# Performance work log

Measured on AMD Instinct MI355X. Metric: run time of the kernel, lower is better.

## Reference

```python
import jax, jax.numpy as jnp
import numpy as np

B = 128      # graphs in batch
NPG = 128    # nodes per graph
F = 256      # num_node_features
D = 192      # d_model
NH = 8       # decoder heads
L = 4        # decoder layers
DFF = 512
DEG = 16     # avg degree
P = 32       # num_patch_nodes
EH = 96      # encoder_hidden = max(D//2, 48)
GH = 4       # GAT heads (layer 1)
EPS = 1e-5


def _init(key, shape, fan_in):
    return jax.random.normal(key, shape, jnp.float32) / np.sqrt(fan_in)


def setup_inputs() -> dict:
    key = jax.random.key(0)
    ks = jax.random.split(key, 40)
    N = B * NPG
    E = N * DEG
    off = jnp.repeat(jnp.arange(B, dtype=jnp.int32) * NPG, E // B)
    src = jax.random.randint(ks[1], (E,), 0, NPG, dtype=jnp.int32) + off
    dst = jax.random.randint(ks[2], (E,), 0, NPG, dtype=jnp.int32) + off
    inp = dict(
        subgraph_x=jax.random.normal(ks[0], (N, F), jnp.float32),
        subgraph_edge_index=jnp.stack([src, dst]),
        target_local_idx=jax.random.randint(ks[3], (B,), 0, NPG, dtype=jnp.int32),
        batch=jnp.repeat(jnp.arange(B, dtype=jnp.int32), NPG),
        num_patch_nodes=P,
    )
    # GAT encoder params (PyG GATConv layout: W [heads*out, in], att [heads, out])
    inp['gat1_w'] = _init(ks[4], (GH * EH, F), F)
    inp['gat1_att_src'] = _init(ks[5], (GH, EH), EH)
    inp['gat1_att_dst'] = _init(ks[6], (GH, EH), EH)
    inp['gat1_b'] = jnp.zeros((GH * EH,), jnp.float32)
    inp['gat2_w'] = _init(ks[7], (D, GH * EH), GH * EH)
    inp['gat2_att_src'] = _init(ks[8], (1, D), D)
    inp['gat2_att_dst'] = _init(ks[9], (1, D), D)
    inp['gat2_b'] = jnp.zeros((D,), jnp.float32)
    # TransformerDecoder layers (stacked over L)
    inp['sa_qkv_w'] = _init(ks[10], (L, 3 * D, D), D)
    inp['sa_qkv_b'] = jnp.zeros((L, 3 * D), jnp.float32)
    inp['sa_out_w'] = _init(ks[11], (L, D, D), D)
    inp['sa_out_b'] = jnp.zeros((L, D), jnp.float32)
    inp['ca_qkv_w'] = _init(ks[12], (L, 3 * D, D), D)
    inp['ca_qkv_b'] = jnp.zeros((L, 3 * D), jnp.float32)
    inp['ca_out_w'] = _init(ks[13], (L, D, D), D)
    inp['ca_out_b'] = jnp.zeros((L, D), jnp.float32)
    inp['ff1_w'] = _init(ks[14], (L, DFF, D), D)
    inp['ff1_b'] = jnp.zeros((L, DFF), jnp.float32)
    inp['ff2_w'] = _init(ks[15], (L, D, DFF), DFF)
    inp['ff2_b'] = jnp.zeros((L, D), jnp.float32)
    inp['ln_g'] = jnp.ones((L, 3, D), jnp.float32)
    inp['ln_b'] = jnp.zeros((L, 3, D), jnp.float32)
    # feature head
    inp['h1_w'] = _init(ks[16], (D, D), D)
    inp['h1_b'] = jnp.zeros((D,), jnp.float32)
    inp['h2_w'] = _init(ks[17], (F, D), D)
    inp['h2_b'] = jnp.zeros((F,), jnp.float32)
    return inp


def _gat(x, src, dst, W, a_src, a_dst, bias, heads, ch, concat):
    # PyG GATConv with add_self_loops=True, negative_slope=0.2, eval mode (no dropout)
    N = x.shape[0]
    xp = (x @ W.T).reshape(N, heads, ch)
    loop = jnp.arange(N, dtype=src.dtype)
    s = jnp.concatenate([src, loop])
    d = jnp.concatenate([dst, loop])
    al_s = (xp * a_src).sum(-1)  # [N, H]
    al_d = (xp * a_dst).sum(-1)
    e = jax.nn.leaky_relu(al_s[s] + al_d[d], 0.2)  # [E+N, H]
    emax = jax.ops.segment_max(e, d, num_segments=N)
    ex = jnp.exp(e - emax[d])
    den = jax.ops.segment_sum(ex, d, num_segments=N)
    coef = ex / (den[d] + 1e-16)
    out = jax.ops.segment_sum(xp[s] * coef[:, :, None], d, num_segments=N)  # [N,H,C]
    out = out.reshape(N, heads * ch) if concat else out.mean(1)
    return out + bias


def _ln(x, g, b):
    m = x.mean(-1, keepdims=True)
    v = ((x - m) ** 2).mean(-1, keepdims=True)
    return (x - m) / jnp.sqrt(v + EPS) * g + b


def _mha(q_in, kv_in, qkv_w, qkv_b, out_w, out_b, causal):
    b, sq, d = q_in.shape
    sk = kv_in.shape[1]
    dh = d // NH
    wq, wk, wv = jnp.split(qkv_w, 3, axis=0)
    bq, bk, bv = jnp.split(qkv_b, 3)
    q = (q_in @ wq.T + bq).reshape(b, sq, NH, dh).transpose(0, 2, 1, 3)
    k = (kv_in @ wk.T + bk).reshape(b, sk, NH, dh).transpose(0, 2, 1, 3)
    v = (kv_in @ wv.T + bv).reshape(b, sk, NH, dh).transpose(0, 2, 1, 3)
    sc = jnp.einsum('bhqd,bhkd->bhqk', q, k) / np.sqrt(dh).astype(np.float32)
    if causal:
        sc = jnp.where(jnp.tril(jnp.ones((sq, sk), bool)), sc, -1e30)
    a = jax.nn.softmax(sc, axis=-1)
    o = jnp.einsum('bhqk,bhkd->bhqd', a, v).transpose(0, 2, 1, 3).reshape(b, sq, d)
    return o @ out_w.T + out_b


def _pe(max_len, d):
    pos = jnp.arange(max_len, dtype=jnp.float32)[:, None]
    div = jnp.exp(jnp.arange(0, d, 2, dtype=jnp.float32) * (-np.log(10000.0) / d))
    pe = jnp.zeros((max_len, d), jnp.float32)
    return pe.at[:, 0::2].set(jnp.sin(pos * div)).at[:, 1::2].set(jnp.cos(pos * div))


def _forward(subgraph_x, gat1_w, gat1_att_src, gat1_att_dst, gat1_b,
             gat2_w, gat2_att_src, gat2_att_dst, gat2_b,
             sa_qkv_w, sa_qkv_b, sa_out_w, sa_out_b,
             ca_qkv_w, ca_qkv_b, ca_out_w, ca_out_b,
             ff1_w, ff1_b, ff2_w, ff2_b, ln_g, ln_b,
             h1_w, h1_b, h2_w, h2_b,
             subgraph_edge_index, target_local_idx, batch, num_patch_nodes):
    src, dst = subgraph_edge_index[0], subgraph_edge_index[1]
    h = jax.nn.elu(_gat(subgraph_x, src, dst, gat1_w, gat1_att_src, gat1_att_dst, gat1_b, GH, EH, True))
    mem = _gat(h, src, dst, gat2_w, gat2_att_src, gat2_att_dst, gat2_b, 1, D, False)
    bsz = target_local_idx.shape[0]
    mem_d = mem.reshape(bsz, -1, D)  # to_dense_batch: equal-sized, sorted graphs -> reshape, mask all-valid
    tgt = mem_d[jnp.arange(bsz), target_local_idx][:, None, :]  # [B,1,D]
    Pn = int(num_patch_nodes)
    pe = _pe(Pn + 1, D)
    feats = []
    adj = jnp.zeros((bsz, Pn + 1, Pn + 1), subgraph_x.dtype)
    for i in range(Pn):
        s = i + 1
        x = tgt + pe[None, :s]  # pos encoding (dropout is eval no-op)
        for l in range(L):
            x = _ln(x + _mha(x, x, sa_qkv_w[l], sa_qkv_b[l], sa_out_w[l], sa_out_b[l], True), ln_g[l, 0], ln_b[l, 0])
            x = _ln(x + _mha(x, mem_d, ca_qkv_w[l], ca_qkv_b[l], ca_out_w[l], ca_out_b[l], False), ln_g[l, 1], ln_b[l, 1])
            ff = jax.nn.gelu(x @ ff1_w[l].T + ff1_b[l], approximate=False) @ ff2_w[l].T + ff2_b[l]
            x = _ln(x + ff, ln_g[l, 2], ln_b[l, 2])
        last = x[:, -1]  # [B,D]
        feats.append(jax.nn.gelu(last @ h1_w.T + h1_b, approximate=False) @ h2_w.T + h2_b)
        cl = jnp.einsum('bsd,bd->bs', x, last)  # connection logits, len s
        adj = adj.at[:, i, Pn].set(cl[:, 0]).at[:, Pn, i].set(cl[:, 0])
        if i > 0:
            adj = adj.at[:, i, :i].set(cl[:, 1:i + 1]).at[:, :i, i].set(cl[:, 1:i + 1])
        tgt = jnp.concatenate([tgt, jax.lax.stop_gradient(last)[:, None]], axis=1)  # .detach() in torch
    adj = jnp.triu(adj, 1)
    adj = adj + jnp.swapaxes(adj, -1, -2)  # symmetric, zero diagonal
    return jnp.stack(feats, axis=1), adj


def reference(subgraph_x, subgraph_edge_index, target_local_idx, batch, num_patch_nodes,
              gat1_w, gat1_att_src, gat1_att_dst, gat1_b,
              gat2_w, gat2_att_src, gat2_att_dst, gat2_b,
              sa_qkv_w, sa_qkv_b, sa_out_w, sa_out_b,
              ca_qkv_w, ca_qkv_b, ca_out_w, ca_out_b,
              ff1_w, ff1_b, ff2_w, ff2_b, ln_g, ln_b,
              h1_w, h1_b, h2_w, h2_b):
    return _forward(subgraph_x, gat1_w, gat1_att_src, gat1_att_dst, gat1_b,
                    gat2_w, gat2_att_src, gat2_att_dst, gat2_b,
                    sa_qkv_w, sa_qkv_b, sa_out_w, sa_out_b,
                    ca_qkv_w, ca_qkv_b, ca_out_w, ca_out_b,
                    ff1_w, ff1_b, ff2_w, ff2_b, ln_g, ln_b,
                    h1_w, h1_b, h2_w, h2_b,
                    subgraph_edge_index, target_local_idx, batch, num_patch_nodes)
```

## Files before the change

### kernel.cpp

```cpp
#include <hip/hip_runtime.h>
#include <hip/hip_bf16.h>
#include <math.h>

#define DEV __device__ __forceinline__
typedef unsigned int u32;
typedef unsigned short u16;

constexpr int NNODES = 16384;
constexpr int NEDGE  = 262144;
constexpr int NEL    = NEDGE + NNODES;
constexpr int FIN    = 256;
constexpr int C1     = 384;
constexpr int DM     = 192;
constexpr int BZ     = 128;
constexpr int NPG_   = 128;
constexpr int LL     = 4;
constexpr int PP     = 32;
constexpr int SM     = 33;
constexpr int DFF_   = 512;

constexpr int PL4     = 52224;
constexpr int OFF4_QKV = 0;
constexpr int OFF4_SAO = 13824;
constexpr int OFF4_CAQ = 18432;
constexpr int OFF4_CAO = 23040;
constexpr int OFF4_FF1 = 27648;
constexpr int OFF4_FF2 = 39936;
constexpr int OFF4_H1  = 4*PL4;
constexpr int OFF4_H2  = OFF4_H1 + 4608;

constexpr size_t O_KVK = 0;
constexpr size_t O_VT  = 6291456;
constexpr size_t O_XP1 = 0;
constexpr size_t O_H   = 6291456;
constexpr size_t O_XP2 = 12582912;
constexpr size_t O_MEM = 15728640;
constexpr size_t O_WP  = 20545536;
constexpr size_t O_PE  = 21424128;
constexpr size_t O_AL1S= O_PE + 6336;
constexpr size_t O_AL1D= O_AL1S + 65536;
constexpr size_t O_AL2S= O_AL1D + 65536;
constexpr size_t O_AL2D= O_AL2S + 16384;
constexpr size_t O_CNT = O_AL2D + 16384;
constexpr size_t O_BASE= O_CNT + 16384;
constexpr size_t O_FILL= O_BASE + 16384;
constexpr size_t O_CSRC= O_FILL + 16384;

DEV float gelu_f(float v) { return 0.5f*v*(1.0f + erff(v*0.7071067811865475f)); }
DEV float bflo(u32 w) { return __uint_as_float(w << 16); }
DEV float bfhi(u32 w) { return __uint_as_float(w & 0xffff0000u); }
DEV float bfu(u16 u)  { return __uint_as_float(((u32)u) << 16); }
DEV u16 bf16u(float a) {
  __hip_bfloat16 h = __float2bfloat16(a);
  return *reinterpret_cast<u16*>(&h);
}
DEV u32 pk2(float a, float b) {
  return (u32)bf16u(a) | ((u32)bf16u(b) << 16);
}
DEV void fma8(float& a, uint4 w, float4 xa, float4 xb) {
  a = fmaf(bflo(w.x), xa.x, a); a = fmaf(bfhi(w.x), xa.y, a);
  a = fmaf(bflo(w.y), xa.z, a); a = fmaf(bfhi(w.y), xa.w, a);
  a = fmaf(bflo(w.z), xb.x, a); a = fmaf(bfhi(w.z), xb.y, a);
  a = fmaf(bflo(w.w), xb.z, a); a = fmaf(bfhi(w.w), xb.w, a);
}
template<int NU4, int STRIDE>
DEV float dotcol(const uint4* __restrict__ col, const float* __restrict__ xv) {
  const float4* x4 = (const float4*)xv;
  float a0 = 0, a1 = 0, a2 = 0, a3 = 0;
  #pragma unroll
  for (int q = 0; q < NU4; ++q) {
    uint4 w = col[(size_t)q*STRIDE];
    if ((q & 3) == 0) fma8(a0, w, x4[2*q], x4[2*q+1]);
    else if ((q & 3) == 1) fma8(a1, w, x4[2*q], x4[2*q+1]);
    else if ((q & 3) == 2) fma8(a2, w, x4[2*q], x4[2*q+1]);
    else fma8(a3, w, x4[2*q], x4[2*q+1]);
  }
  return (a0+a1)+(a2+a3);
}
template<int N> struct WB { uint4 w[N]; };
template<int N, int STRIDE>
DEV void wissue(WB<N>& r, const uint4* __restrict__ col) {
  #pragma unroll
  for (int q = 0; q < N; ++q) r.w[q] = col[(size_t)q*STRIDE];
}
template<int N>
DEV float wuse(const WB<N>& r, const float* __restrict__ xv) {
  const float4* x4 = (const float4*)xv;
  float a0 = 0, a1 = 0, a2 = 0, a3 = 0;
  #pragma unroll
  for (int q = 0; q < N; ++q) {
    float4 xa = x4[2*q], xb = x4[2*q+1];
    if ((q & 3) == 0) fma8(a0, r.w[q], xa, xb);
    else if ((q & 3) == 1) fma8(a1, r.w[q], xa, xb);
    else if ((q & 3) == 2) fma8(a2, r.w[q], xa, xb);
    else fma8(a3, r.w[q], xa, xb);
  }
  return (a0+a1)+(a2+a3);
}

__global__ void zero_kernel(float* adj, int* cnt, int* fill) {
  int i = blockIdx.x*256 + threadIdx.x;
  if (i < BZ*SM*SM) adj[i] = 0.f;
  if (i < NNODES) { cnt[i] = 0; fill[i] = 0; }
}

__global__ void pe_kernel(float* pe) {
  int idx = blockIdx.x*256 + threadIdx.x;
  if (idx >= SM*DM) return;
  int p = idx / DM, d = idx % DM;
  int i2 = d >> 1;
  float div = __expf((float)(2*i2) * (-9.210340371976184f / (float)DM));
  float a = (float)p * div;
  pe[idx] = (d & 1) ? cosf(a) : sinf(a);
}

__global__ void pack_kernel(const float* __restrict__ W, uint4* __restrict__ P, int N, int K) {
  int idx = blockIdx.x*256 + threadIdx.x;
  if (idx >= N*(K>>3)) return;
  int o = idx % N, kq = idx / N;
  const float* r = W + (size_t)o*K + 8*kq;
  uint4 u;
  u.x = pk2(r[0], r[1]); u.y = pk2(r[2], r[3]);
  u.z = pk2(r[4], r[5]); u.w = pk2(r[6], r[7]);
  P[idx] = u;
}

template<int BMODE, bool BF16OUT>
__global__ __launch_bounds__(256) void gemm_nt(const float* __restrict__ A,
    const float* __restrict__ W, const float* __restrict__ bias,
    float* __restrict__ Cf, __hip_bfloat16* __restrict__ Cb, int M, int N, int K)
{
  __shared__ float As[16][68];
  __shared__ float Ws[16][68];
  const int bm = blockIdx.y*64, bn = blockIdx.x*64;
  const int t = threadIdx.x, tx = t & 15, ty = t >> 4;
  float acc[4][4] = {};
  for (int k0 = 0; k0 < K; k0 += 16) {
    #pragma unroll
    for (int i = 0; i < 4; ++i) {
      int idx = t + i*256, kk = idx & 15, m = idx >> 4;
      As[kk][m] = A[(size_t)(bm+m)*K + k0+kk];
      Ws[kk][m] = W[(size_t)(bn+m)*K + k0+kk];
    }
    __syncthreads();
    #pragma unroll
    for (int kk = 0; kk < 16; ++kk) {
      const float4 a4 = *(const float4*)&As[kk][ty*4];
      const float4 b4 = *(const float4*)&Ws[kk][tx*4];
      const float av[4] = {a4.x,a4.y,a4.z,a4.w};
      const float bv[4] = {b4.x,b4.y,b4.z,b4.w};
      #pragma unroll
      for (int i = 0; i < 4; ++i)
        #pragma unroll
        for (int j = 0; j < 4; ++j)
          acc[i][j] = fmaf(av[i], bv[j], acc[i][j]);
    }
    __syncthreads();
  }
  #pragma unroll
  for (int i = 0; i < 4; ++i) {
    const int m = bm + ty*4 + i;
    #pragma unroll
    for (int j = 0; j < 4; ++j) {
      const int n = bn + tx*4 + j;
      float v = acc[i][j];
      if (BMODE == 1) v += bias[n];
      if (BMODE == 2) v += bias[m];
      if (BF16OUT) Cb[(size_t)m*N + n] = __float2bfloat16(v);
      else         Cf[(size_t)m*N + n] = v;
    }
  }
}

template<int HEADS, int CH>
__global__ void al_kernel(const float* __restrict__ xp, const float* __restrict__ asrc,
                          const float* __restrict__ adst, float* als, float* ald) {
  int idx = blockIdx.x*256 + threadIdx.x;
  if (idx >= NNODES*HEADS) return;
  int n = idx / HEADS, h = idx % HEADS;
  const float* row = xp + (size_t)n*(HEADS*CH) + h*CH;
  float s = 0, d = 0;
  for (int c = 0; c < CH; ++c) { float v = row[c]; s = fmaf(v, asrc[h*CH+c], s); d = fmaf(v, adst[h*CH+c], d); }
  als[idx] = s; ald[idx] = d;
}

__global__ void count_kernel(const int* __restrict__ dst, int* cnt) {
  int e = blockIdx.x*256 + threadIdx.x;
  if (e < NEDGE) atomicAdd(&cnt[dst[e]], 1);
}

__global__ __launch_bounds__(1024) void scan_kernel(const int* __restrict__ cnt, int* base) {
  __shared__ int tot[1024];
  int t = threadIdx.x;
  int local[16]; int s = 0;
  #pragma unroll
  for (int i = 0; i < 16; ++i) { int v = cnt[t*16+i] + 1; local[i] = s; s += v; }
  tot[t] = s; __syncthreads();
  if (t == 0) { int r = 0; for (int i = 0; i < 1024; ++i) { int v = tot[i]; tot[i] = r; r += v; } }
  __syncthreads();
  int off = tot[t];
  #pragma unroll
  for (int i = 0; i < 16; ++i) base[t*16+i] = off + local[i];
}

__global__ void scatter_kernel(const int* __restrict__ src, const int* __restrict__ dst,
                               const int* __restrict__ base, int* fill, int* csrc) {
  int e = blockIdx.x*256 + threadIdx.x;
  if (e < NEDGE) {
    int d = dst[e];
    int p = atomicAdd(&fill[d], 1);
    csrc[base[d] + p] = src[e];
  } else if (e < NEL) {
    int n = e - NEDGE;
    int p = atomicAdd(&fill[n], 1);
    csrc[base[n] + p] = n;
  }
}

template<int HEADS, int CH, bool ELU>
__global__ __launch_bounds__(128) void agg_kernel(const float* __restrict__ xp,
    const float* __restrict__ als, const float* __restrict__ ald,
    const int* __restrict__ cnt, const int* __restrict__ base, const int* __restrict__ csrc,
    const float* __restrict__ bias, float* __restrict__ out)
{
  constexpr int CO = HEADS*CH;
  constexpr int MAXD = 128;
  int n = blockIdx.x, t = threadIdx.x;
  int deg = cnt[n] + 1, st = base[n];
  if (deg > MAXD) deg = MAXD;
  __shared__ int   srcs[MAXD];
  __shared__ float ex[MAXD][HEADS];
  __shared__ float den[HEADS];
  for (int j = t; j < deg; j += 128) srcs[j] = csrc[st + j];
  __syncthreads();
  for (int idx = t; idx < deg*HEADS; idx += 128) {
    int j = idx / HEADS, h = idx % HEADS;
    float e = als[srcs[j]*HEADS + h] + ald[n*HEADS + h];
    ex[j][h] = (e > 0.f) ? e : 0.2f*e;
  }
  __syncthreads();
  if (t < HEADS) {
    float m = -1e30f;
    for (int j = 0; j < deg; ++j) m = fmaxf(m, ex[j][t]);
    float s = 0;
    for (int j = 0; j < deg; ++j) { float v = __expf(ex[j][t]-m); ex[j][t] = v; s += v; }
    den[t] = 1.0f/(s + 1e-16f);
  }
  __syncthreads();
  for (int c = t; c < CO; c += 128) {
    int h = c / CH;
    float acc = 0;
    for (int j = 0; j < deg; ++j) acc = fmaf(ex[j][h], xp[(size_t)srcs[j]*CO + c], acc);
    float v = acc*den[h] + bias[c];
    if (ELU) v = (v > 0.f) ? v : (__expf(v) - 1.0f);
    out[(size_t)n*CO + c] = v;
  }
}

__global__ __launch_bounds__(1024, 1) void decode_kernel(
    const float* __restrict__ mem, const u16* __restrict__ kvk, const u16* __restrict__ vT,
    const uint4* __restrict__ wp, const float* __restrict__ pe,
    const int* __restrict__ tgt_idx,
    const float* __restrict__ saqkvb, const float* __restrict__ saoutb,
    const float* __restrict__ caqkvb, const float* __restrict__ caoutb,
    const float* __restrict__ ff1b, const float* __restrict__ ff2b,
    const float* __restrict__ lng, const float* __restrict__ lnb,
    const float* __restrict__ h1b, const float* __restrict__ h2b,
    float* __restrict__ feats, float* __restrict__ adj)
{
  const int b = blockIdx.x, t = threadIdx.x;
  const int wv = t >> 6, lane = t & 63;
  __shared__ u16   ksa16[4*33*194];
  __shared__ u16   vsa16[4*33*194];
  __shared__ float lasts[SM][193];
  __shared__ __align__(16) float x[DM];
  __shared__ __align__(16) float qkv[DM];
  __shared__ __align__(16) float attno[DM];
  __shared__ __align__(16) float hid[DFF_];
  __shared__ float prob[33*9 + 7];
  __shared__ float cprob[128*9 + 2];
  __shared__ __align__(16) float psA[1152];
  __shared__ float painv[8], cainv[8], red[16];
  const float scl = 0.2041241452319315f;
  const float* tgt0 = mem + ((size_t)b*NPG_ + tgt_idx[b])*DM;
  const uint4* kvk4 = (const uint4*)kvk;

  const int qks = t / 576, qcol = t - qks*576;
  const int k4s = t >> 9,  o512 = t & 511;
  const int ks4 = (t < 768) ? t/192 : 0;
  const int o192 = t - ((t < 768) ? (t/192)*192 : 0);
  const int ks2h = t >> 8, o256 = t & 255;
  const int caj = t >> 3, cah = t & 7;

  WB<3> rCAK;

  auto ln_ps4 = [&](const float* g, const float* be) {
    float v = 0.f;
    if (t < DM) v = x[t] + ((psA[t]+psA[192+t]) + (psA[384+t]+psA[576+t]));
    float s = v, q = v*v;
    #pragma unroll
    for (int o = 32; o; o >>= 1) { s += __shfl_down(s, o, 64); q += __shfl_down(q, o, 64); }
    if (lane == 0 && wv < 3) { red[wv] = s; red[8+wv] = q; }
    __syncthreads();
    float S = red[0]+red[1]+red[2];
    float Q = red[8]+red[9]+red[10];
    float mu = S*(1.f/DM), var = Q*(1.f/DM) - mu*mu;
    float rstd = rsqrtf(var + 1e-5f);
    if (t < DM) x[t] = (v-mu)*rstd*g[t] + be[t];
    __syncthreads();
  };

  if (t < DM) x[t] = tgt0[t] + pe[t];
  __syncthreads();

  for (int i = 0; i < PP; ++i) {
    for (int l = 0; l < LL; ++l) {
      const uint4* WL = wp + (size_t)l*PL4;
      {
        psA[t] = (qks ? 0.f : saqkvb[l*576 + qcol]) + dotcol<12,576>(WL + OFF4_QKV + qks*12*576 + qcol, x + 96*qks);
        if (t < 128)
          psA[1024 + t] = dotcol<12,576>(WL + OFF4_QKV + 12*576 + 448 + t, x + 96);
      }
      wissue<3,1>(rCAK, kvk4 + ((size_t)l*NNODES + b*NPG_ + caj)*24 + cah*3);
      __syncthreads();
      if (t < 576) {
        float a = psA[t] + psA[576 + t];
        if (t < 192)      qkv[t] = a;
        else if (t < 384) ksa16[(l*33 + i)*194 + (t-192)] = bf16u(a);
        else              vsa16[(l*33 + i)*194 + (t-384)] = bf16u(a);
      }
      __syncthreads();
      if (wv < 8) {
        float s = -1e30f;
        if (lane <= i) {
          const u32* kr = (const u32*)ksa16 + ((size_t)l*33 + lane)*97 + wv*12;
          float a0 = 0, a1 = 0;
          #pragma unroll
          for (int c = 0; c < 12; c += 2) {
            u32 w0 = kr[c], w1 = kr[c+1];
            a0 = fmaf(bflo(w0), qkv[wv*24 + 2*c],   a0);
            a0 = fmaf(bfhi(w0), qkv[wv*24 + 2*c+1], a0);
            a1 = fmaf(bflo(w1), qkv[wv*24 + 2*c+2], a1);
            a1 = fmaf(bfhi(w1), qkv[wv*24 + 2*c+3], a1);
          }
          s = (a0+a1) * scl;
        }
        float m = s;
        #pragma unroll
        for (int o2 = 32; o2; o2 >>= 1) m = fmaxf(m, __shfl_xor(m, o2, 64));
        float e = (lane <= i) ? __expf(s - m) : 0.f;
        float sm = e;
        #pragma unroll
        for (int o2 = 32; o2; o2 >>= 1) sm += __shfl_xor(sm, o2, 64);
        if (lane <= i) prob[lane*9 + wv] = e;
        if (lane == 0) painv[wv] = 1.0f / sm;
      }
      __syncthreads();
      if (t < DM) {
        int hh = t / 24;
        const u16* vr = vsa16 + (size_t)l*33*194 + t;
        float a0 = 0, a1 = 0;
        for (int j = 0; j + 1 <= i; j += 2) {
          a0 = fmaf(prob[j*9 + hh],     bfu(vr[(size_t)j*194]),     a0);
          a1 = fmaf(prob[(j+1)*9 + hh], bfu(vr[(size_t)(j+1)*194]), a1);
        }
        if (!(i & 1)) a0 = fmaf(prob[i*9 + hh], bfu(vr[(size_t)i*194]), a0);
        attno[t] = (a0 + a1) * painv[hh];
      }
      __syncthreads();
      if (t < 768)
        psA[t] = (ks4 ? 0.f : saoutb[l*DM + o192]) + dotcol<6,192>(WL + OFF4_SAO + ks4*6*192 + o192, attno + 48*ks4);
      __syncthreads();
      ln_ps4(lng + (l*3+0)*DM, lnb + (l*3+0)*DM);
      if (t < 768)
        psA[t] = (ks4 ? 0.f : caqkvb[l*3*DM + o192]) + dotcol<6,192>(WL + OFF4_CAQ + ks4*6*192 + o192, x + 48*ks4);
      __syncthreads();
      {
        float4 qv4[6];
        const int cbase = cah*24;
        #pragma unroll
        for (int o2 = 0; o2 < 6; ++o2) {
          float4 v;
          int c0 = cbase + 4*o2;
          v.x = (psA[c0+0]+psA[192+c0+0]) + (psA[384+c0+0]+psA[576+c0+0]);
          v.y = (psA[c0+1]+psA[192+c0+1]) + (psA[384+c0+1]+psA[576+c0+1]);
          v.z = (psA[c0+2]+psA[192+c0+2]) + (psA[384+c0+2]+psA[576+c0+2]);
          v.w = (psA[c0+3]+psA[192+c0+3]) + (psA[384+c0+3]+psA[576+c0+3]);
          qv4[o2] = v;
        }
        cprob[caj*9 + cah] = scl * wuse<3>(rCAK, (const float*)qv4);
      }
      __syncthreads();
      if (wv < 8) {
        float s0 = cprob[lane*9 + wv], s1 = cprob[(lane+64)*9 + wv];
        float m = fmaxf(s0, s1);
        #pragma unroll
        for (int o2 = 32; o2; o2 >>= 1) m = fmaxf(m, __shfl_xor(m, o2, 64));
        float e0 = __expf(s0-m), e1 = __expf(s1-m);
        float sm = e0+e1;
        #pragma unroll
        for (int o2 = 32; o2; o2 >>= 1) sm += __shfl_xor(sm, o2, 64);
        cprob[lane*9 + wv] = e0; cprob[(lane+64)*9 + wv] = e1;
        if (lane == 0) cainv[wv] = 1.0f / sm;
      }
      __syncthreads();
      if (t < DM) {
        int hh = t / 24;
        const uint4* v4 = (const uint4*)(vT + ((size_t)l*DM + t)*NNODES + b*NPG_);
        float a0 = 0, a1 = 0;
        #pragma unroll
        for (int q = 0; q < 16; ++q) {
          uint4 w = v4[q];
          int j0 = q*8;
          a0 = fmaf(cprob[(j0+0)*9 + hh], bflo(w.x), a0);
          a1 = fmaf(cprob[(j0+1)*9 + hh], bfhi(w.x), a1);
          a0 = fmaf(cprob[(j0+2)*9 + hh], bflo(w.y), a0);
          a1 = fmaf(cprob[(j0+3)*9 + hh], bfhi(w.y), a1);
          a0 = fmaf(cprob[(j0+4)*9 + hh], bflo(w.z), a0);
          a1 = fmaf(cprob[(j0+5)*9 + hh], bfhi(w.z), a1);
          a0 = fmaf(cprob[(j0+6)*9 + hh], bflo(w.w), a0);
          a1 = fmaf(cprob[(j0+7)*9 + hh], bfhi(w.w), a1);
        }
        attno[t] = (a0 + a1) * cainv[hh];
      }
      __syncthreads();
      if (t < 768)
        psA[t] = (ks4 ? 0.f : caoutb[l*DM + o192]) + dotcol<6,192>(WL + OFF4_CAO + ks4*6*192 + o192, attno + 48*ks4);
      __syncthreads();
      ln_ps4(lng + (l*3+1)*DM, lnb + (l*3+1)*DM);
      psA[t] = (k4s ? 0.f : ff1b[l*DFF_ + o512]) + dotcol<12,512>(WL + OFF4_FF1 + k4s*12*512 + o512, x + 96*k4s);
      __syncthreads();
      if (t < DFF_) hid[t] = gelu_f(psA[t] + psA[512+t]);
      __syncthreads();
      if (t < 768)
        psA[t] = (ks4 ? 0.f : ff2b[l*DM + o192]) + dotcol<16,192>(WL + OFF4_FF2 + ks4*16*192 + o192, hid + 128*ks4);
      __syncthreads();
      ln_ps4(lng + (l*3+2)*DM, lnb + (l*3+2)*DM);
    }
    if (t < 768)
      psA[t] = (ks4 ? 0.f : h1b[o192]) + dotcol<6,192>(wp + OFF4_H1 + ks4*6*192 + o192, x + 48*ks4);
    __syncthreads();
    if (t < DM) {
      hid[t] = gelu_f((psA[t]+psA[192+t]) + (psA[384+t]+psA[576+t]));
      lasts[i][t] = x[t];
    }
    __syncthreads();
    psA[t] = (ks2h ? 0.f : h2b[o256]) + dotcol<6,256>(wp + OFF4_H2 + ks2h*6*256 + o256, hid + 48*ks2h);
    __syncthreads();
    if (t < 256) {
      feats[((size_t)b*PP + i)*256 + t] = (psA[t]+psA[256+t]) + (psA[512+t]+psA[768+t]);
    } else if (t < 289 && (t - 256) <= i) {
      int jj = t - 256;
      float a = 0.f;
      for (int d = 0; d < DM; ++d) a = fmaf(lasts[jj][d], lasts[i][d], a);
      if (jj == 0) {
        adj[((size_t)b*SM + i)*SM + 32] = a;
        adj[((size_t)b*SM + 32)*SM + i] = a;
      } else {
        adj[((size_t)b*SM + jj-1)*SM + i] = a;
        adj[((size_t)b*SM + i)*SM + jj-1] = a;
      }
    } else if (t >= 512 && t < 704) {
      int d = t - 512;
      x[d] = lasts[i][d] + pe[(i+1)*DM + d];
    }
    __syncthreads();
  }
}

extern "C" void kernel_launch(void* const* d_in, const int* in_sizes, int n_in,
                              void* d_out, int out_size, void* d_ws, size_t ws_size,
                              hipStream_t stream) {
  (void)in_sizes; (void)n_in; (void)out_size; (void)ws_size;
  const float* x_in    = (const float*)d_in[0];
  const int*   ei      = (const int*)d_in[1];
  const int*   tgt_idx = (const int*)d_in[2];
  const float* gat1_w  = (const float*)d_in[5];
  const float* g1as    = (const float*)d_in[6];
  const float* g1ad    = (const float*)d_in[7];
  const float* g1b     = (const float*)d_in[8];
  const float* gat2_w  = (const float*)d_in[9];
  const float* g2as    = (const float*)d_in[10];
  const float* g2ad    = (const float*)d_in[11];
  const float* g2b     = (const float*)d_in[12];
  const float* saqkvw  = (const float*)d_in[13];
  const float* saqkvb  = (const float*)d_in[14];
  const float* saoutw  = (const float*)d_in[15];
  const float* saoutb  = (const float*)d_in[16];
  const float* caqkvw  = (const float*)d_in[17];
  const float* caqkvb  = (const float*)d_in[18];
  const float* caoutw  = (const float*)d_in[19];
  const float* caoutb  = (const float*)d_in[20];
  const float* ff1w    = (const float*)d_in[21];
  const float* ff1b    = (const float*)d_in[22];
  const float* ff2w    = (const float*)d_in[23];
  const float* ff2b    = (const float*)d_in[24];
  const float* lng     = (const float*)d_in[25];
  const float* lnb     = (const float*)d_in[26];
  const float* h1w     = (const float*)d_in[27];
  const float* h1b     = (const float*)d_in[28];
  const float* h2w     = (const float*)d_in[29];
  const float* h2b     = (const float*)d_in[30];

  float* ws  = (float*)d_ws;
  float* out = (float*)d_out;
  float* adj = out + (size_t)BZ*PP*256;

  const int* src = ei;
  const int* dst = ei + NEDGE;

  int* cnt  = (int*)(ws + O_CNT);
  int* base = (int*)(ws + O_BASE);
  int* fill = (int*)(ws + O_FILL);
  int* csrc = (int*)(ws + O_CSRC);

  hipLaunchKernelGGL(zero_kernel, dim3(545), dim3(256), 0, stream, adj, cnt, fill);

  hipLaunchKernelGGL((gemm_nt<0,false>), dim3(C1/64, NNODES/64), dim3(256), 0, stream,
                     x_in, gat1_w, (const float*)nullptr, ws + O_XP1, (__hip_bfloat16*)nullptr,
                     NNODES, C1, FIN);
  hipLaunchKernelGGL((al_kernel<4,96>), dim3(NNODES*4/256), dim3(256), 0, stream,
                     ws+O_XP1, g1as, g1ad, ws+O_AL1S, ws+O_AL1D);
  hipLaunchKernelGGL(count_kernel, dim3(NEDGE/256), dim3(256), 0, stream, dst, cnt);
  hipLaunchKernelGGL(scan_kernel, dim3(1), dim3(1024), 0, stream, cnt, base);
  hipLaunchKernelGGL(scatter_kernel, dim3(NEL/256), dim3(256), 0, stream, src, dst, base, fill, csrc);
  hipLaunchKernelGGL((agg_kernel<4,96,true>), dim3(NNODES), dim3(128), 0, stream,
                     ws+O_XP1, ws+O_AL1S, ws+O_AL1D, cnt, base, csrc, g1b, ws+O_H);

  hipLaunchKernelGGL((gemm_nt<0,false>), dim3(DM/64, NNODES/64), dim3(256), 0, stream,
                     ws+O_H, gat2_w, (const float*)nullptr, ws+O_XP2, (__hip_bfloat16*)nullptr,
                     NNODES, DM, C1);
  hipLaunchKernelGGL((al_kernel<1,192>), dim3(NNODES/256), dim3(256), 0, stream,
                     ws+O_XP2, g2as, g2ad, ws+O_AL2S, ws+O_AL2D);
  hipLaunchKernelGGL((agg_kernel<1,192,false>), dim3(NNODES), dim3(128), 0, stream,
                     ws+O_XP2, ws+O_AL2S, ws+O_AL2D, cnt, base, csrc, g2b, ws+O_MEM);

  uint4* wp = (uint4*)(ws + O_WP);
  auto PK = [&](const float* Wsrc, int off_u4, int N, int K) {
    hipLaunchKernelGGL(pack_kernel, dim3((N*(K/8)+255)/256), dim3(256), 0, stream,
                       Wsrc, wp + off_u4, N, K);
  };
  for (int l = 0; l < LL; ++l) {
    PK(saqkvw + (size_t)l*110592, l*PL4 + OFF4_QKV, 576, 192);
    PK(saoutw + (size_t)l*36864,  l*PL4 + OFF4_SAO, 192, 192);
    PK(caqkvw + (size_t)l*110592, l*PL4 + OFF4_CAQ, 192, 192);
    PK(caoutw + (size_t)l*36864,  l*PL4 + OFF4_CAO, 192, 192);
    PK(ff1w   + (size_t)l*98304,  l*PL4 + OFF4_FF1, 512, 192);
    PK(ff2w   + (size_t)l*98304,  l*PL4 + OFF4_FF2, 192, 512);
  }
  PK(h1w, OFF4_H1, 192, 192);
  PK(h2w, OFF4_H2, 256, 192);

  hipLaunchKernelGGL(pe_kernel, dim3((SM*DM+255)/256), dim3(256), 0, stream, ws+O_PE);

  __hip_bfloat16* kvk = (__hip_bfloat16*)(ws + O_KVK);
  __hip_bfloat16* vT  = (__hip_bfloat16*)(ws + O_VT);
  for (int l = 0; l < LL; ++l) {
    hipLaunchKernelGGL((gemm_nt<1,true>), dim3(DM/64, NNODES/64), dim3(256), 0, stream,
                       ws+O_MEM, caqkvw + (size_t)l*110592 + (size_t)192*192,
                       caqkvb + l*576 + 192, (float*)nullptr,
                       kvk + (size_t)l*NNODES*DM, NNODES, DM, DM);
    hipLaunchKernelGGL((gemm_nt<2,true>), dim3(NNODES/64, DM/64), dim3(256), 0, stream,
                       caqkvw + (size_t)l*110592 + (size_t)2*192*192, ws+O_MEM,
                       caqkvb + l*576 + 384, (float*)nullptr,
                       vT + (size_t)l*DM*NNODES, DM, NNODES, DM);
  }

  hipLaunchKernelGGL(decode_kernel, dim3(BZ), dim3(1024), 0, stream,
                     ws+O_MEM, (const u16*)kvk, (const u16*)vT, wp, ws+O_PE, tgt_idx,
                     saqkvb, saoutb, caqkvb, caoutb, ff1b, ff2b, lng, lnb, h1b, h2b,
                     out, adj);
}
```

Baseline: 4.356 ms.

## Move output head MLP and adjacency out of serial decode loop into batched kernels

```diff
diff --git a/kernel.cpp b/kernel.cpp
--- a/kernel.cpp
+++ b/kernel.cpp
@@ -26,8 +26,6 @@
 constexpr int OFF4_CAO = 23040;
 constexpr int OFF4_FF1 = 27648;
 constexpr int OFF4_FF2 = 39936;
-constexpr int OFF4_H1  = 4*PL4;
-constexpr int OFF4_H2  = OFF4_H1 + 4608;
 
 constexpr size_t O_KVK = 0;
 constexpr size_t O_VT  = 6291456;
@@ -45,6 +43,7 @@
 constexpr size_t O_BASE= O_CNT + 16384;
 constexpr size_t O_FILL= O_BASE + 16384;
 constexpr size_t O_CSRC= O_FILL + 16384;
+constexpr size_t O_LASTS=O_CSRC + 278528;
 
 DEV float gelu_f(float v) { return 0.5f*v*(1.0f + erff(v*0.7071067811865475f)); }
 DEV float bflo(u32 w) { return __uint_as_float(w << 16); }
@@ -125,7 +124,7 @@
   P[idx] = u;
 }
 
-template<int BMODE, bool BF16OUT>
+template<int BMODE, bool BF16OUT, bool GELU = false>
 __global__ __launch_bounds__(256) void gemm_nt(const float* __restrict__ A,
     const float* __restrict__ W, const float* __restrict__ bias,
     float* __restrict__ Cf, __hip_bfloat16* __restrict__ Cb, int M, int N, int K)
@@ -166,6 +165,7 @@
       float v = acc[i][j];
       if (BMODE == 1) v += bias[n];
       if (BMODE == 2) v += bias[m];
+      if (GELU) v = gelu_f(v);
       if (BF16OUT) Cb[(size_t)m*N + n] = __float2bfloat16(v);
       else         Cf[(size_t)m*N + n] = v;
     }
@@ -257,6 +257,22 @@
   }
 }
 
+__global__ void adj_kernel(const float* __restrict__ lastsG, float* __restrict__ adj) {
+  int b = blockIdx.x, i = blockIdx.y, jj = threadIdx.x;
+  if (jj > i) return;
+  const float* li = lastsG + ((size_t)b*PP + i)*DM;
+  const float* lj = lastsG + ((size_t)b*PP + jj)*DM;
+  float a = 0.f;
+  for (int d = 0; d < DM; ++d) a = fmaf(lj[d], li[d], a);
+  if (jj == 0) {
+    adj[((size_t)b*SM + i)*SM + 32] = a;
+    adj[((size_t)b*SM + 32)*SM + i] = a;
+  } else {
+    adj[((size_t)b*SM + jj-1)*SM + i] = a;
+    adj[((size_t)b*SM + i)*SM + jj-1] = a;
+  }
+}
+
 __global__ __launch_bounds__(1024, 1) void decode_kernel(
     const float* __restrict__ mem, const u16* __restrict__ kvk, const u16* __restrict__ vT,
     const uint4* __restrict__ wp, const float* __restrict__ pe,
@@ -265,14 +281,12 @@
     const float* __restrict__ caqkvb, const float* __restrict__ caoutb,
     const float* __restrict__ ff1b, const float* __restrict__ ff2b,
     const float* __restrict__ lng, const float* __restrict__ lnb,
-    const float* __restrict__ h1b, const float* __restrict__ h2b,
-    float* __restrict__ feats, float* __restrict__ adj)
+    float* __restrict__ lastsG)
 {
   const int b = blockIdx.x, t = threadIdx.x;
   const int wv = t >> 6, lane = t & 63;
   __shared__ u16   ksa16[4*33*194];
   __shared__ u16   vsa16[4*33*194];
-  __shared__ float lasts[SM][193];
   __shared__ __align__(16) float x[DM];
   __shared__ __align__(16) float qkv[DM];
   __shared__ __align__(16) float attno[DM];
@@ -289,7 +303,6 @@
   const int k4s = t >> 9,  o512 = t & 511;
   const int ks4 = (t < 768) ? t/192 : 0;
   const int o192 = t - ((t < 768) ? (t/192)*192 : 0);
-  const int ks2h = t >> 8, o256 = t & 255;
   const int caj = t >> 3, cah = t & 7;
 
   WB<3> rCAK;
@@ -437,32 +450,10 @@
       __syncthreads();
       ln_ps4(lng + (l*3+2)*DM, lnb + (l*3+2)*DM);
     }
-    if (t < 768)
-      psA[t] = (ks4 ? 0.f : h1b[o192]) + dotcol<6,192>(wp + OFF4_H1 + ks4*6*192 + o192, x + 48*ks4);
-    __syncthreads();
     if (t < DM) {
-      hid[t] = gelu_f((psA[t]+psA[192+t]) + (psA[384+t]+psA[576+t]));
-      lasts[i][t] = x[t];
-    }
-    __syncthreads();
-    psA[t] = (ks2h ? 0.f : h2b[o256]) + dotcol<6,256>(wp + OFF4_H2 + ks2h*6*256 + o256, hid + 48*ks2h);
-    __syncthreads();
-    if (t < 256) {
-      feats[((size_t)b*PP + i)*256 + t] = (psA[t]+psA[256+t]) + (psA[512+t]+psA[768+t]);
-    } else if (t < 289 && (t - 256) <= i) {
-      int jj = t - 256;
-      float a = 0.f;
-      for (int d = 0; d < DM; ++d) a = fmaf(lasts[jj][d], lasts[i][d], a);
-      if (jj == 0) {
-        adj[((size_t)b*SM + i)*SM + 32] = a;
-        adj[((size_t)b*SM + 32)*SM + i] = a;
-      } else {
-        adj[((size_t)b*SM + jj-1)*SM + i] = a;
-        adj[((size_t)b*SM + i)*SM + jj-1] = a;
-      }
-    } else if (t >= 512 && t < 704) {
-      int d = t - 512;
-      x[d] = lasts[i][d] + pe[(i+1)*DM + d];
+      float xv = x[t];
+      lastsG[((size_t)b*PP + i)*DM + t] = xv;
+      if (i + 1 < PP) x[t] = xv + pe[(i+1)*DM + t];
     }
     __syncthreads();
   }
@@ -513,6 +504,8 @@
   int* base = (int*)(ws + O_BASE);
   int* fill = (int*)(ws + O_FILL);
   int* csrc = (int*)(ws + O_CSRC);
+  float* lastsG = ws + O_LASTS;
+  float* hidG   = ws + O_XP2;
 
   hipLaunchKernelGGL(zero_kernel, dim3(545), dim3(256), 0, stream, adj, cnt, fill);
 
@@ -548,8 +541,6 @@
     PK(ff1w   + (size_t)l*98304,  l*PL4 + OFF4_FF1, 512, 192);
     PK(ff2w   + (size_t)l*98304,  l*PL4 + OFF4_FF2, 192, 512);
   }
-  PK(h1w, OFF4_H1, 192, 192);
-  PK(h2w, OFF4_H2, 256, 192);
 
   hipLaunchKernelGGL(pe_kernel, dim3((SM*DM+255)/256), dim3(256), 0, stream, ws+O_PE);
 
@@ -568,6 +559,14 @@
 
   hipLaunchKernelGGL(decode_kernel, dim3(BZ), dim3(1024), 0, stream,
                      ws+O_MEM, (const u16*)kvk, (const u16*)vT, wp, ws+O_PE, tgt_idx,
-                     saqkvb, saoutb, caqkvb, caoutb, ff1b, ff2b, lng, lnb, h1b, h2b,
-                     out, adj);
-}
+                     saqkvb, saoutb, caqkvb, caoutb, ff1b, ff2b, lng, lnb,
+                     lastsG);
+
+  hipLaunchKernelGGL((gemm_nt<1,false,true>), dim3(DM/64, (BZ*PP)/64), dim3(256), 0, stream,
+                     lastsG, h1w, h1b, hidG, (__hip_bfloat16*)nullptr,
+                     BZ*PP, DM, DM);
+  hipLaunchKernelGGL((gemm_nt<1,false,false>), dim3(256/64, (BZ*PP)/64), dim3(256), 0, stream,
+                     hidG, h2w, h2b, out, (__hip_bfloat16*)nullptr,
+                     BZ*PP, 256, DM);
+  hipLaunchKernelGGL(adj_kernel, dim3(BZ, PP), dim3(64), 0, stream, lastsG, adj);
+}
```

New measurement: 3.783 ms. 13.1% less time.
